# Kernel tuning notes

Hardware: AMD Instinct MI355X
Metric: run time of the kernel (lower is better)

Reference implementation:

```python
import jax, jax.numpy as jnp
import numpy as np

N, E, D, H, Z = 20000, 320000, 512, 512, 128
SCALING_FACTOR = 1.0


def setup_inputs() -> dict:
    key = jax.random.key(0)
    ks = jax.random.split(key, 12)
    def glorot(k, fi, fo):
        lim = float(np.sqrt(6.0 / (fi + fo)))
        return jax.random.uniform(k, (fi, fo), jnp.float32, -lim, lim)
    return {
        "x": jax.random.normal(ks[0], (N, D), jnp.float32),
        "edge_index": jax.random.randint(ks[1], (2, E), 0, N, jnp.int32),
        "eps": jax.random.normal(ks[2], (N, Z), jnp.float32),
        "W1": glorot(ks[3], D, H), "b1": jnp.zeros((H,), jnp.float32),
        "W2": glorot(ks[4], H, H), "b2": jnp.zeros((H,), jnp.float32),
        "Wmu": glorot(ks[5], H, Z), "bmu": jnp.zeros((Z,), jnp.float32),
        "Wlv": glorot(ks[6], H, Z), "blv": jnp.zeros((Z,), jnp.float32),
    }


def reference(x, edge_index, eps, W1, b1, W2, b2, Wmu, bmu, Wlv, blv):
    n = x.shape[0]
    src, dst = edge_index[0], edge_index[1]
    # GCN symmetric normalization with added self-loops (PyG GCNConv default)
    deg = jax.ops.segment_sum(jnp.ones(src.shape[0], x.dtype), dst, num_segments=n) + 1.0
    dinv = jax.lax.rsqrt(deg)                      # deg^{-1/2}, deg >= 1
    edge_coef = dinv[src] * dinv[dst]              # [E]
    self_coef = dinv * dinv                        # [N] self-loop weight

    def gcn(h, W, b):
        h = h @ W                                  # linear first, then propagate
        agg = jax.ops.segment_sum(h[src] * edge_coef[:, None], dst, num_segments=n)
        return agg + self_coef[:, None] * h + b

    # hidden layer 0: relu -> dropout(eval=identity) -> L2 normalize * scaling
    h = jax.nn.relu(gcn(x, W1, b1))
    h = h / jnp.maximum(jnp.linalg.norm(h, axis=1, keepdims=True), 1e-12) * SCALING_FACTOR
    # hidden layer 1 (last): relu only
    h = jax.nn.relu(gcn(h, W2, b2))
    # GaussianSample: GCN heads for mu / log_var, reparameterized sample
    mu = gcn(h, Wmu, bmu)
    log_var = gcn(h, Wlv, blv)
    z = mu + eps * jnp.exp(0.5 * log_var)
    return z, mu, log_var
```

## Files before the change

### kernel.cpp

```cpp
#include <hip/hip_runtime.h>

typedef __bf16 bf16x8 __attribute__((ext_vector_type(8)));
typedef __bf16 bf16x4 __attribute__((ext_vector_type(4)));
typedef float  f32x4  __attribute__((ext_vector_type(4)));
typedef float  f32x2  __attribute__((ext_vector_type(2)));

#define GLDS16(g, l) __builtin_amdgcn_global_load_lds( \
    (const __attribute__((address_space(1))) void*)(g), \
    (__attribute__((address_space(3))) void*)(l), 16, 0, 0)

#define FP8_SCALE 64.0f
#define FP8_INV   (1.0f / 64.0f)

__device__ __forceinline__ unsigned char fp8_of_f32(float v) {
  return (unsigned char)(__builtin_amdgcn_cvt_pk_fp8_f32(v, v, 0, false) & 0xff);
}
__device__ __forceinline__ void dec4(unsigned int u, float* o) {
  f32x2 lo = __builtin_amdgcn_cvt_pk_f32_fp8(u, false);
  f32x2 hi = __builtin_amdgcn_cvt_pk_f32_fp8(u, true);
  o[0] = lo[0]; o[1] = lo[1]; o[2] = hi[0]; o[3] = hi[1];
}


#define CNT_BLKS 640
#define WT_BLKS  640

__global__ __launch_bounds__(256) void prep_kernel(
    const int* __restrict__ dstv, int* __restrict__ cnt, int E,
    const float* __restrict__ x, __bf16* __restrict__ xb,
    const float* __restrict__ W1, const float* __restrict__ W2,
    const float* __restrict__ Wmu, const float* __restrict__ Wlv,
    __bf16* __restrict__ w1t, __bf16* __restrict__ w2t, __bf16* __restrict__ wct) {
  const int b = blockIdx.x;
  if (b < CNT_BLKS) {
    int idx = b * 256 + threadIdx.x;
    for (int e = idx; e < E; e += CNT_BLKS * 256) atomicAdd(&cnt[dstv[e]], 1);
  } else if (b < CNT_BLKS + WT_BLKS) {
    __shared__ float tile[32][33];
    int t = b - CNT_BLKS;
    const float* S; __bf16* D; int kt, ntl, drow, snw;
    if (t < 256)      { S = W1;  D = w1t; kt = t & 15;        ntl = t >> 4;        drow = ntl * 32;       snw = 512; }
    else if (t < 512) { int u = t - 256; S = W2;  D = w2t; kt = u & 15; ntl = u >> 4; drow = ntl * 32;       snw = 512; }
    else if (t < 576) { int u = t - 512; S = Wmu; D = wct; kt = u & 15; ntl = u >> 4; drow = ntl * 32;       snw = 128; }
    else              { int u = t - 576; S = Wlv; D = wct; kt = u & 15; ntl = u >> 4; drow = 128 + ntl * 32; snw = 128; }
    const int k0 = kt * 32, n0 = ntl * 32;
    const int r = threadIdx.x >> 5, c = threadIdx.x & 31;
    #pragma unroll
    for (int p = 0; p < 4; p++)
      tile[r + p * 8][c] = S[(k0 + r + p * 8) * snw + n0 + c];
    __syncthreads();
    #pragma unroll
    for (int p = 0; p < 4; p++)
      D[(drow + r + p * 8) * 512 + k0 + c] = (__bf16)tile[c][r + p * 8];
  } else {
    int id = (b - CNT_BLKS - WT_BLKS) * 256 + threadIdx.x;
    if (id < 2560000) {
      float4 v = ((const float4*)x)[id];
      bf16x4 o; o[0] = (__bf16)v.x; o[1] = (__bf16)v.y; o[2] = (__bf16)v.z; o[3] = (__bf16)v.w;
      ((bf16x4*)xb)[id] = o;
    }
  }
}


__global__ __launch_bounds__(1024) void scan1_kernel(const int* __restrict__ cnt,
                                                     int* __restrict__ rowptr,
                                                     float* __restrict__ dinv,
                                                     int* __restrict__ bsum, int n) {
  __shared__ int wsum[16];
  const int t = threadIdx.x, b = blockIdx.x;
  const int gid = b * 1024 + t;
  const int lane = t & 63, w = t >> 6;
  int val = (gid < n) ? cnt[gid] : 0;
  if (gid < n) dinv[gid] = rsqrtf((float)val + 1.0f);
  int incl = val;
  #pragma unroll
  for (int off = 1; off < 64; off <<= 1) {
    int u = __shfl_up(incl, off);
    if (lane >= off) incl += u;
  }
  if (lane == 63) wsum[w] = incl;
  __syncthreads();
  if (w == 0) {
    int v = (lane < 16) ? wsum[lane] : 0;
    int iv = v;
    #pragma unroll
    for (int off = 1; off < 16; off <<= 1) {
      int u = __shfl_up(iv, off);
      if (lane >= off) iv += u;
    }
    if (lane < 16) wsum[lane] = iv - v;
    if (lane == 15) bsum[b] = iv;
  }
  __syncthreads();
  if (gid < n) rowptr[gid] = wsum[w] + incl - val;
}

__global__ __launch_bounds__(1024) void scan23_kernel(int* __restrict__ rowptr,
                                                      const int* __restrict__ bsum,
                                                      int n, int nb) {
  __shared__ int off_s;
  const int b = blockIdx.x;
  if (threadIdx.x == 0) {
    int run = 0;
    for (int i = 0; i < b; i++) run += bsum[i];
    off_s = run;
    if (b == nb - 1) rowptr[n] = run + bsum[b];
  }
  __syncthreads();
  int gid = b * 1024 + threadIdx.x;
  if (gid < n) rowptr[gid] += off_s;
}


__device__ __forceinline__ void gemm_tile(int orig, int nb,
                                          const __bf16* __restrict__ A,
                                          const __bf16* __restrict__ Bt,
                                          unsigned char* __restrict__ C,
                                          int M, int N, int K, int ntiles_n) {
  __shared__ __align__(16) __bf16 sA[2][128 * 32];
  __shared__ __align__(16) __bf16 sB[2][128 * 32];
  const int q = nb >> 3, r = nb & 7;
  const int xcd = orig & 7, sub = orig >> 3;
  const int pos = (xcd < r) ? (xcd * (q + 1) + sub) : (r * (q + 1) + (xcd - r) * q + sub);
  const int m0 = (pos / ntiles_n) * 128, n0 = (pos % ntiles_n) * 128;

  const int tid = threadIdx.x;
  const int wave = tid >> 6, lane = tid & 63;
  const int wr = wave >> 1, wc = wave & 1;
  f32x4 acc[4][4] = {};
  const int srow = lane >> 2;
  const int sg   = (lane & 3) ^ ((srow >> 1) & 3);
  const int nt = K >> 5;

  auto STAGE = [&](int bb, int k0) {
    #pragma unroll
    for (int c = 0; c < 2; ++c) {
      int chunk = wave * 2 + c;
      int row = chunk * 16 + srow;
      int ga = m0 + row; if (ga >= M) ga = M - 1;
      GLDS16(A  + (long)ga * K         + k0 + sg * 8, sA[bb] + chunk * 512);
      GLDS16(Bt + (long)(n0 + row) * K + k0 + sg * 8, sB[bb] + chunk * 512);
    }
  };

  STAGE(0, 0);
  for (int t = 0; t < nt; ++t) {
    const int cur = t & 1;
    if (t + 1 < nt) {
      STAGE(cur ^ 1, (t + 1) << 5);
      asm volatile("s_waitcnt vmcnt(4)" ::: "memory");
    } else {
      asm volatile("s_waitcnt vmcnt(0)" ::: "memory");
    }
    __builtin_amdgcn_s_barrier();
    __builtin_amdgcn_sched_barrier(0);

    const int fr = lane & 15, gbase = lane >> 4;
    const int gs = gbase ^ ((fr >> 1) & 3);
    bf16x8 af[4], bfr[4];
    #pragma unroll
    for (int mi = 0; mi < 4; mi++)
      af[mi] = *(const bf16x8*)(sA[cur] + (wr * 64 + mi * 16 + fr) * 32 + gs * 8);
    #pragma unroll
    for (int ni = 0; ni < 4; ni++)
      bfr[ni] = *(const bf16x8*)(sB[cur] + (wc * 64 + ni * 16 + fr) * 32 + gs * 8);
    #pragma unroll
    for (int mi = 0; mi < 4; mi++)
      #pragma unroll
      for (int ni = 0; ni < 4; ni++)
        acc[mi][ni] = __builtin_amdgcn_mfma_f32_16x16x32_bf16(af[mi], bfr[ni], acc[mi][ni], 0, 0, 0);
    asm volatile("s_waitcnt lgkmcnt(0)" ::: "memory");
    __builtin_amdgcn_sched_barrier(0);
    __builtin_amdgcn_s_barrier();
  }

  const int crow0 = (lane >> 4) * 4, ccol = lane & 15;
  #pragma unroll
  for (int mi = 0; mi < 4; mi++)
    #pragma unroll
    for (int ni = 0; ni < 4; ni++)
      #pragma unroll
      for (int r2 = 0; r2 < 4; r2++) {
        int row = m0 + wr * 64 + mi * 16 + crow0 + r2;
        if (row < M)
          C[(long)row * N + n0 + wc * 64 + ni * 16 + ccol] =
              fp8_of_f32(acc[mi][ni][r2] * FP8_SCALE);
      }
}

__global__ __launch_bounds__(256, 4) void gemm_bt(const __bf16* __restrict__ A,
                                                  const __bf16* __restrict__ Bt,
                                                  unsigned char* __restrict__ C,
                                                  int M, int N, int K, int ntiles_n, int ngb) {
  gemm_tile(blockIdx.x, ngb, A, Bt, C, M, N, K, ntiles_n);
}

__global__ __launch_bounds__(256, 4) void gemm1_fill_kernel(
    const __bf16* __restrict__ A, const __bf16* __restrict__ Bt,
    unsigned char* __restrict__ C, int M, int N, int K, int ntiles_n, int ngb,
    const int* __restrict__ src, const int* __restrict__ dstv,
    const int* __restrict__ rowptr, int* __restrict__ cur,
    const float* __restrict__ dinv, int2* __restrict__ csr_pack, int E) {
  if (blockIdx.x < (unsigned)ngb) {
    gemm_tile(blockIdx.x, ngb, A, Bt, C, M, N, K, ntiles_n);
  } else {
    int idx = (blockIdx.x - ngb) * 256 + threadIdx.x;
    int stride = (gridDim.x - ngb) * 256;
    for (int e = idx; e < E; e += stride) {
      int s = src[e], d = dstv[e];
      int slot = rowptr[d] + atomicAdd(&cur[d], 1);
      int2 p; p.x = s; p.y = __float_as_int(dinv[s] * dinv[d] * FP8_INV);
      csr_pack[slot] = p;
    }
  }
}


template<int EPL> struct LSel;
template<> struct LSel<8> { typedef uint2 T; };
template<> struct LSel<4> { typedef unsigned int T; };

template<int EPL, int MODE>
__global__ __launch_bounds__(512) void prop_kernel(
    const unsigned char* __restrict__ Cin, const int* __restrict__ rowptr,
    const int2* __restrict__ csr_pack,
    const float* __restrict__ dinv, const float* __restrict__ bias,
    const float* __restrict__ bmu, const float* __restrict__ blv,
    const float* __restrict__ eps,
    __bf16* __restrict__ hout, float* __restrict__ zout, int n) {
  constexpr int F = EPL * 64;
  typedef typename LSel<EPL>::T VecT;
  const int lane = threadIdx.x & 63;
  const int i = blockIdx.x * (blockDim.x >> 6) + (threadIdx.x >> 6);
  if (i >= n) return;
  const unsigned char* __restrict__ Clane = Cin + lane * EPL;

  auto decAll = [&](VecT v, float* o) {
    if constexpr (EPL == 8) { dec4(v.x, o); dec4(v.y, o + 4); }
    else                    { dec4(v, o); }
  };

  float acc[EPL];
  {
    const float di = dinv[i];
    const float sc = di * di * FP8_INV;
    VecT v = *(const VecT*)(Clane + (size_t)i * F);
    float dv[EPL];
    decAll(v, dv);
    #pragma unroll
    for (int j = 0; j < EPL; j++) acc[j] = sc * dv[j];
  }
  int e = rowptr[i];
  const int e1 = rowptr[i + 1];
  for (; e + 8 <= e1; e += 8) {
    int2 p[8];
    #pragma unroll
    for (int q = 0; q < 8; q++) p[q] = csr_pack[e + q];
    VecT v[8];
    #pragma unroll
    for (int q = 0; q < 8; q++) v[q] = *(const VecT*)(Clane + (size_t)p[q].x * F);
    #pragma unroll
    for (int q = 0; q < 8; q++) {
      float c = __int_as_float(p[q].y);
      float dv[EPL];
      decAll(v[q], dv);
      #pragma unroll
      for (int j = 0; j < EPL; j++) acc[j] += c * dv[j];
    }
  }
  for (; e + 4 <= e1; e += 4) {
    int2 p[4];
    #pragma unroll
    for (int q = 0; q < 4; q++) p[q] = csr_pack[e + q];
    VecT v[4];
    #pragma unroll
    for (int q = 0; q < 4; q++) v[q] = *(const VecT*)(Clane + (size_t)p[q].x * F);
    #pragma unroll
    for (int q = 0; q < 4; q++) {
      float c = __int_as_float(p[q].y);
      float dv[EPL];
      decAll(v[q], dv);
      #pragma unroll
      for (int j = 0; j < EPL; j++) acc[j] += c * dv[j];
    }
  }
  for (; e < e1; ++e) {
    int2 p = csr_pack[e];
    float c = __int_as_float(p.y);
    VecT v = *(const VecT*)(Clane + (size_t)p.x * F);
    float dv[EPL];
    decAll(v, dv);
    #pragma unroll
    for (int j = 0; j < EPL; j++) acc[j] += c * dv[j];
  }

  if constexpr (MODE == 0 || MODE == 1) {
    float ss = 0.f;
    #pragma unroll
    for (int j = 0; j < EPL; j++) {
      acc[j] += bias[lane * EPL + j];
      acc[j] = fmaxf(acc[j], 0.f);
      ss += acc[j] * acc[j];
    }
    float scale = 1.f;
    if constexpr (MODE == 0) {
      #pragma unroll
      for (int off = 32; off > 0; off >>= 1) ss += __shfl_xor(ss, off);
      scale = 1.f / fmaxf(sqrtf(ss), 1e-12f);
    }
    bf16x8 o;
    #pragma unroll
    for (int j = 0; j < EPL; j++) o[j] = (__bf16)(acc[j] * scale);
    *(bf16x8*)(hout + (size_t)i * 512 + lane * EPL) = o;
  } else {
    const bool ismu = lane < 32;
    const int cb4 = (ismu ? lane : lane - 32) * 4;
    float v[4];
    #pragma unroll
    for (int j = 0; j < 4; j++) v[j] = acc[j] + (ismu ? bmu[cb4 + j] : blv[cb4 + j]);
    const size_t NZ = (size_t)n * 128;
    float* dstp = ismu ? (zout + NZ + (size_t)i * 128 + cb4)
                       : (zout + 2 * NZ + (size_t)i * 128 + cb4);
    float4 st; st.x = v[0]; st.y = v[1]; st.z = v[2]; st.w = v[3];
    *(float4*)dstp = st;
    float ov[4];
    #pragma unroll
    for (int j = 0; j < 4; j++) ov[j] = __shfl_xor(v[j], 32);
    if (ismu) {
      float4 ev = *(const float4*)(eps + (size_t)i * 128 + cb4);
      float4 zs;
      zs.x = v[0] + ev.x * expf(0.5f * ov[0]);
      zs.y = v[1] + ev.y * expf(0.5f * ov[1]);
      zs.z = v[2] + ev.z * expf(0.5f * ov[2]);
      zs.w = v[3] + ev.w * expf(0.5f * ov[3]);
      *(float4*)(zout + (size_t)i * 128 + cb4) = zs;
    }
  }
}


extern "C" void kernel_launch(void* const* d_in, const int* in_sizes, int n_in,
                              void* d_out, int out_size, void* d_ws, size_t ws_size,
                              hipStream_t stream) {
  const float* x   = (const float*)d_in[0];
  const int*   ei  = (const int*)d_in[1];
  const float* eps = (const float*)d_in[2];
  const float* W1  = (const float*)d_in[3];
  const float* b1  = (const float*)d_in[4];
  const float* W2  = (const float*)d_in[5];
  const float* b2  = (const float*)d_in[6];
  const float* Wmu = (const float*)d_in[7];
  const float* bmu = (const float*)d_in[8];
  const float* Wlv = (const float*)d_in[9];
  const float* blv = (const float*)d_in[10];
  float* out = (float*)d_out;

  const int N = 20000, E = 320000, D = 512, H = 512, Z = 128;
  const int* src = ei;
  const int* dst = ei + E;
  const int NB = (N + 1023) / 1024;

  char* p = (char*)d_ws;
  auto alloc = [&](size_t bytes) { char* r = p; p += (bytes + 255) & ~(size_t)255; return r; };
  int*    cnt      = (int*)alloc((size_t)N * 4);
  int*    cur      = (int*)alloc((size_t)N * 4);
  int*    rowptr   = (int*)alloc((size_t)(N + 1) * 4);
  float*  dinv     = (float*)alloc((size_t)N * 4);
  int*    bsum     = (int*)alloc((size_t)NB * 4);
  int2*   csr_pack = (int2*)alloc((size_t)E * 8);
  __bf16* xb  = (__bf16*)alloc((size_t)N * D * 2);
  __bf16* hb  = (__bf16*)alloc((size_t)N * H * 2);
  unsigned char* cb = (unsigned char*)alloc((size_t)N * H);
  __bf16* w1t = (__bf16*)alloc((size_t)D * H * 2);
  __bf16* w2t = (__bf16*)alloc((size_t)H * H * 2);
  __bf16* wct = (__bf16*)alloc((size_t)2 * Z * H * 2);

  hipMemsetAsync(cnt, 0, ((size_t)N * 4 + 255 & ~(size_t)255) + (size_t)N * 4, stream);

  prep_kernel<<<CNT_BLKS + WT_BLKS + 10000, 256, 0, stream>>>(
      dst, cnt, E, x, xb, W1, W2, Wmu, Wlv, w1t, w2t, wct);
  scan1_kernel<<<NB, 1024, 0, stream>>>(cnt, rowptr, dinv, bsum, N);
  scan23_kernel<<<NB, 1024, 0, stream>>>(rowptr, bsum, N, NB);

  const int NGB1 = ((N + 127) / 128) * (H / 128);
  gemm1_fill_kernel<<<NGB1 + 1250, 256, 0, stream>>>(
      xb, w1t, cb, N, H, D, H / 128, NGB1,
      src, dst, rowptr, cur, dinv, csr_pack, E);
  prop_kernel<8, 0><<<2500, 512, 0, stream>>>(cb, rowptr, csr_pack, dinv,
                                              b1, nullptr, nullptr, nullptr, hb, nullptr, N);
  gemm_bt<<<NGB1, 256, 0, stream>>>(hb, w2t, cb, N, H, H, H / 128, NGB1);
  prop_kernel<8, 1><<<2500, 512, 0, stream>>>(cb, rowptr, csr_pack, dinv,
                                              b2, nullptr, nullptr, nullptr, xb, nullptr, N);
  const int NGB3 = ((N + 127) / 128) * ((2 * Z) / 128);
  gemm_bt<<<NGB3, 256, 0, stream>>>(xb, wct, cb, N, 2 * Z, H, (2 * Z) / 128, NGB3);
  prop_kernel<4, 2><<<2500, 512, 0, stream>>>(cb, rowptr, csr_pack, dinv,
                                              nullptr, bmu, blv, eps, nullptr, out, N);
}
```

Before: 182.2 us.

## Fuse all stages into one cooperative persistent kernel with grid syncs

Replaces the sequence of separate launches (prep, count, scans, gemms, propagations) with one cooperative mega-kernel that loops persistently over work and separates phases with grid.sync, keeping a multi-kernel fallback. The memset is folded into the prep phase. The intent is to remove per-launch overhead and inter-kernel gaps. In exchange, occupancy is capped at the cooperative grid size (at most 1024 blocks), the GEMM runs as grid-strided tiles, grid-wide barriers add their own cost, and the edge fill may no longer overlap with the GEMM if the grid is too small.

```diff
diff --git a/kernel.cpp b/kernel.cpp
--- a/kernel.cpp
+++ b/kernel.cpp
@@ -1,4 +1,7 @@
 #include <hip/hip_runtime.h>
+#include <hip/hip_cooperative_groups.h>
+
+namespace cg = cooperative_groups;
 
 typedef __bf16 bf16x8 __attribute__((ext_vector_type(8)));
 typedef __bf16 bf16x4 __attribute__((ext_vector_type(4)));
@@ -12,6 +15,13 @@
 #define FP8_SCALE 64.0f
 #define FP8_INV   (1.0f / 64.0f)
 
+#define MN    20000
+#define ME    320000
+#define NGB1  628
+#define NGB3  314
+#define SCB   80
+#define SMEM_B (32768 + 32)
+
 __device__ __forceinline__ unsigned char fp8_of_f32(float v) {
   return (unsigned char)(__builtin_amdgcn_cvt_pk_fp8_f32(v, v, 0, false) & 0xff);
 }
@@ -21,105 +31,27 @@
   o[0] = lo[0]; o[1] = lo[1]; o[2] = hi[0]; o[3] = hi[1];
 }
 
-
-#define CNT_BLKS 640
-#define WT_BLKS  640
-
-__global__ __launch_bounds__(256) void prep_kernel(
-    const int* __restrict__ dstv, int* __restrict__ cnt, int E,
-    const float* __restrict__ x, __bf16* __restrict__ xb,
-    const float* __restrict__ W1, const float* __restrict__ W2,
-    const float* __restrict__ Wmu, const float* __restrict__ Wlv,
-    __bf16* __restrict__ w1t, __bf16* __restrict__ w2t, __bf16* __restrict__ wct) {
-  const int b = blockIdx.x;
-  if (b < CNT_BLKS) {
-    int idx = b * 256 + threadIdx.x;
-    for (int e = idx; e < E; e += CNT_BLKS * 256) atomicAdd(&cnt[dstv[e]], 1);
-  } else if (b < CNT_BLKS + WT_BLKS) {
-    __shared__ float tile[32][33];
-    int t = b - CNT_BLKS;
-    const float* S; __bf16* D; int kt, ntl, drow, snw;
-    if (t < 256)      { S = W1;  D = w1t; kt = t & 15;        ntl = t >> 4;        drow = ntl * 32;       snw = 512; }
-    else if (t < 512) { int u = t - 256; S = W2;  D = w2t; kt = u & 15; ntl = u >> 4; drow = ntl * 32;       snw = 512; }
-    else if (t < 576) { int u = t - 512; S = Wmu; D = wct; kt = u & 15; ntl = u >> 4; drow = ntl * 32;       snw = 128; }
-    else              { int u = t - 576; S = Wlv; D = wct; kt = u & 15; ntl = u >> 4; drow = 128 + ntl * 32; snw = 128; }
-    const int k0 = kt * 32, n0 = ntl * 32;
-    const int r = threadIdx.x >> 5, c = threadIdx.x & 31;
-    #pragma unroll
-    for (int p = 0; p < 4; p++)
-      tile[r + p * 8][c] = S[(k0 + r + p * 8) * snw + n0 + c];
-    __syncthreads();
-    #pragma unroll
-    for (int p = 0; p < 4; p++)
-      D[(drow + r + p * 8) * 512 + k0 + c] = (__bf16)tile[c][r + p * 8];
-  } else {
-    int id = (b - CNT_BLKS - WT_BLKS) * 256 + threadIdx.x;
-    if (id < 2560000) {
-      float4 v = ((const float4*)x)[id];
-      bf16x4 o; o[0] = (__bf16)v.x; o[1] = (__bf16)v.y; o[2] = (__bf16)v.z; o[3] = (__bf16)v.w;
-      ((bf16x4*)xb)[id] = o;
-    }
-  }
-}
-
-
-__global__ __launch_bounds__(1024) void scan1_kernel(const int* __restrict__ cnt,
-                                                     int* __restrict__ rowptr,
-                                                     float* __restrict__ dinv,
-                                                     int* __restrict__ bsum, int n) {
-  __shared__ int wsum[16];
-  const int t = threadIdx.x, b = blockIdx.x;
-  const int gid = b * 1024 + t;
-  const int lane = t & 63, w = t >> 6;
-  int val = (gid < n) ? cnt[gid] : 0;
-  if (gid < n) dinv[gid] = rsqrtf((float)val + 1.0f);
-  int incl = val;
-  #pragma unroll
-  for (int off = 1; off < 64; off <<= 1) {
-    int u = __shfl_up(incl, off);
-    if (lane >= off) incl += u;
-  }
-  if (lane == 63) wsum[w] = incl;
-  __syncthreads();
-  if (w == 0) {
-    int v = (lane < 16) ? wsum[lane] : 0;
-    int iv = v;
-    #pragma unroll
-    for (int off = 1; off < 16; off <<= 1) {
-      int u = __shfl_up(iv, off);
-      if (lane >= off) iv += u;
-    }
-    if (lane < 16) wsum[lane] = iv - v;
-    if (lane == 15) bsum[b] = iv;
-  }
-  __syncthreads();
-  if (gid < n) rowptr[gid] = wsum[w] + incl - val;
-}
-
-__global__ __launch_bounds__(1024) void scan23_kernel(int* __restrict__ rowptr,
-                                                      const int* __restrict__ bsum,
-                                                      int n, int nb) {
-  __shared__ int off_s;
-  const int b = blockIdx.x;
-  if (threadIdx.x == 0) {
-    int run = 0;
-    for (int i = 0; i < b; i++) run += bsum[i];
-    off_s = run;
-    if (b == nb - 1) rowptr[n] = run + bsum[b];
-  }
-  __syncthreads();
-  int gid = b * 1024 + threadIdx.x;
-  if (gid < n) rowptr[gid] += off_s;
-}
+struct MegaArgs {
+  const int* src; const int* dstv;
+  int* cnt; int* cur; int* rowptr; float* dinv; int* bsum;
+  int2* csr_pack;
+  const float* x; __bf16* xb;
+  const float* W1; const float* W2; const float* Wmu; const float* Wlv;
+  __bf16* w1t; __bf16* w2t; __bf16* wct;
+  unsigned char* cb; __bf16* hb;
+  const float* b1; const float* b2; const float* bmu; const float* blv;
+  const float* eps; float* zout;
+};
 
 
 __device__ __forceinline__ void gemm_tile(int orig, int nb,
                                           const __bf16* __restrict__ A,
                                           const __bf16* __restrict__ Bt,
                                           unsigned char* __restrict__ C,
-                                          int M, int N, int K, int ntiles_n) {
-  __shared__ __align__(16) __bf16 sA[2][128 * 32];
-  __shared__ __align__(16) __bf16 sB[2][128 * 32];
+                                          int M, int N, int K, int ntiles_n,
+                                          char* smem) {
+  __bf16* sA[2] = { (__bf16*)smem, (__bf16*)smem + 128 * 32 };
+  __bf16* sB[2] = { (__bf16*)smem + 2 * 128 * 32, (__bf16*)smem + 3 * 128 * 32 };
   const int q = nb >> 3, r = nb & 7;
   const int xcd = orig & 7, sub = orig >> 3;
   const int pos = (xcd < r) ? (xcd * (q + 1) + sub) : (r * (q + 1) + (xcd - r) * q + sub);
@@ -189,31 +121,118 @@
       }
 }
 
-__global__ __launch_bounds__(256, 4) void gemm_bt(const __bf16* __restrict__ A,
-                                                  const __bf16* __restrict__ Bt,
-                                                  unsigned char* __restrict__ C,
-                                                  int M, int N, int K, int ntiles_n, int ngb) {
-  gemm_tile(blockIdx.x, ngb, A, Bt, C, M, N, K, ntiles_n);
-}
-
-__global__ __launch_bounds__(256, 4) void gemm1_fill_kernel(
-    const __bf16* __restrict__ A, const __bf16* __restrict__ Bt,
-    unsigned char* __restrict__ C, int M, int N, int K, int ntiles_n, int ngb,
-    const int* __restrict__ src, const int* __restrict__ dstv,
-    const int* __restrict__ rowptr, int* __restrict__ cur,
-    const float* __restrict__ dinv, int2* __restrict__ csr_pack, int E) {
-  if (blockIdx.x < (unsigned)ngb) {
-    gemm_tile(blockIdx.x, ngb, A, Bt, C, M, N, K, ntiles_n);
+
+__device__ void ph_prep(const MegaArgs& a, char* smem) {
+  float (*tile)[33] = (float(*)[33])smem;
+  const int b = blockIdx.x, t = threadIdx.x;
+  const int G = gridDim.x;
+  const int gtid = b * 256 + t, gsz = G * 256;
+  for (int i = gtid; i < MN; i += gsz) { a.cnt[i] = 0; a.cur[i] = 0; }
+  for (int tt = b; tt < 640; tt += G) {
+    const float* S; __bf16* D; int kt, ntl, drow, snw;
+    if (tt < 256)      { S = a.W1;  D = a.w1t; kt = tt & 15;  ntl = tt >> 4; drow = ntl * 32;       snw = 512; }
+    else if (tt < 512) { int u = tt - 256; S = a.W2;  D = a.w2t; kt = u & 15; ntl = u >> 4; drow = ntl * 32;       snw = 512; }
+    else if (tt < 576) { int u = tt - 512; S = a.Wmu; D = a.wct; kt = u & 15; ntl = u >> 4; drow = ntl * 32;       snw = 128; }
+    else               { int u = tt - 576; S = a.Wlv; D = a.wct; kt = u & 15; ntl = u >> 4; drow = 128 + ntl * 32; snw = 128; }
+    const int k0 = kt * 32, n0 = ntl * 32;
+    const int r = t >> 5, c = t & 31;
+    #pragma unroll
+    for (int p = 0; p < 4; p++)
+      tile[r + p * 8][c] = S[(k0 + r + p * 8) * snw + n0 + c];
+    __syncthreads();
+    #pragma unroll
+    for (int p = 0; p < 4; p++)
+      D[(drow + r + p * 8) * 512 + k0 + c] = (__bf16)tile[c][r + p * 8];
+    __syncthreads();
+  }
+  for (int id = gtid; id < 2560000; id += gsz) {
+    float4 v = ((const float4*)a.x)[id];
+    bf16x4 o; o[0] = (__bf16)v.x; o[1] = (__bf16)v.y; o[2] = (__bf16)v.z; o[3] = (__bf16)v.w;
+    ((bf16x4*)a.xb)[id] = o;
+  }
+}
+
+__device__ void ph_count(const MegaArgs& a) {
+  const int gtid = blockIdx.x * 256 + threadIdx.x, gsz = gridDim.x * 256;
+  for (int e = gtid; e < ME; e += gsz) atomicAdd(&a.cnt[a.dstv[e]], 1);
+}
+
+__device__ void ph_scan1(const MegaArgs& a, char* smem) {
+  int* ssc = (int*)(smem + 32768);
+  const int t = threadIdx.x;
+  const int lane = t & 63, w = t >> 6;
+  for (int sb = blockIdx.x; sb < SCB; sb += gridDim.x) {
+    const int gid = sb * 256 + t;
+    int val = (gid < MN) ? a.cnt[gid] : 0;
+    if (gid < MN) a.dinv[gid] = rsqrtf((float)val + 1.0f);
+    int incl = val;
+    #pragma unroll
+    for (int off = 1; off < 64; off <<= 1) {
+      int u = __shfl_up(incl, off);
+      if (lane >= off) incl += u;
+    }
+    if (lane == 63) ssc[w] = incl;
+    __syncthreads();
+    if (t == 0) {
+      int s = 0;
+      #pragma unroll
+      for (int j = 0; j < 4; j++) { int tmp = ssc[j]; ssc[j] = s; s += tmp; }
+      a.bsum[sb] = s;
+    }
+    __syncthreads();
+    if (gid < MN) a.rowptr[gid] = ssc[w] + incl - val;
+    __syncthreads();
+  }
+}
+
+__device__ void ph_scan23(const MegaArgs& a, char* smem) {
+  int* ssc = (int*)(smem + 32768);
+  const int t = threadIdx.x;
+  for (int sb = blockIdx.x; sb < SCB; sb += gridDim.x) {
+    if (t == 0) {
+      int run = 0;
+      for (int i = 0; i < sb; i++) run += a.bsum[i];
+      ssc[4] = run;
+      if (sb == SCB - 1) a.rowptr[MN] = run + a.bsum[sb];
+    }
+    __syncthreads();
+    const int gid = sb * 256 + t;
+    if (gid < MN) a.rowptr[gid] += ssc[4];
+    __syncthreads();
+  }
+}
+
+__device__ __forceinline__ void fill_edges(const MegaArgs& a, int idx, int stride) {
+  for (int e = idx; e < ME; e += stride) {
+    int s = a.src[e], d = a.dstv[e];
+    int slot = a.rowptr[d] + atomicAdd(&a.cur[d], 1);
+    int2 pp; pp.x = s; pp.y = __float_as_int(a.dinv[s] * a.dinv[d] * FP8_INV);
+    a.csr_pack[slot] = pp;
+  }
+}
+
+__device__ void ph_gemm1_fill(const MegaArgs& a, char* smem) {
+  const int G = gridDim.x, b = blockIdx.x;
+  if (G >= NGB1 + 64) {
+    if (b < NGB1)
+      gemm_tile(b, NGB1, a.xb, a.w1t, a.cb, MN, 512, 512, 4, smem);
+    else
+      fill_edges(a, (b - NGB1) * 256 + threadIdx.x, (G - NGB1) * 256);
   } else {
-    int idx = (blockIdx.x - ngb) * 256 + threadIdx.x;
-    int stride = (gridDim.x - ngb) * 256;
-    for (int e = idx; e < E; e += stride) {
-      int s = src[e], d = dstv[e];
-      int slot = rowptr[d] + atomicAdd(&cur[d], 1);
-      int2 p; p.x = s; p.y = __float_as_int(dinv[s] * dinv[d] * FP8_INV);
-      csr_pack[slot] = p;
-    }
-  }
+    for (int tl = b; tl < NGB1; tl += G)
+      gemm_tile(tl, NGB1, a.xb, a.w1t, a.cb, MN, 512, 512, 4, smem);
+    fill_edges(a, b * 256 + threadIdx.x, G * 256);
+  }
+}
+
+__device__ void ph_gemm2(const MegaArgs& a, char* smem) {
+  for (int tl = blockIdx.x; tl < NGB1; tl += gridDim.x)
+    gemm_tile(tl, NGB1, a.hb, a.w2t, a.cb, MN, 512, 512, 4, smem);
+}
+
+__device__ void ph_gemm3(const MegaArgs& a, char* smem) {
+  for (int tl = blockIdx.x; tl < NGB3; tl += gridDim.x)
+    gemm_tile(tl, NGB3, a.xb, a.wct, a.cb, MN, 256, 512, 2, smem);
 }
 
 
@@ -222,18 +241,13 @@
 template<> struct LSel<4> { typedef unsigned int T; };
 
 template<int EPL, int MODE>
-__global__ __launch_bounds__(512) void prop_kernel(
-    const unsigned char* __restrict__ Cin, const int* __restrict__ rowptr,
-    const int2* __restrict__ csr_pack,
-    const float* __restrict__ dinv, const float* __restrict__ bias,
-    const float* __restrict__ bmu, const float* __restrict__ blv,
-    const float* __restrict__ eps,
-    __bf16* __restrict__ hout, float* __restrict__ zout, int n) {
+__device__ void prop_phase(const MegaArgs& a, const unsigned char* __restrict__ Cin,
+                           const float* __restrict__ bias, __bf16* __restrict__ hout) {
   constexpr int F = EPL * 64;
   typedef typename LSel<EPL>::T VecT;
   const int lane = threadIdx.x & 63;
-  const int i = blockIdx.x * (blockDim.x >> 6) + (threadIdx.x >> 6);
-  if (i >= n) return;
+  const int w = threadIdx.x >> 6;
+  const int nw = gridDim.x * 4;
   const unsigned char* __restrict__ Clane = Cin + lane * EPL;
 
   auto decAll = [&](VecT v, float* o) {
@@ -241,125 +255,140 @@
     else                    { dec4(v, o); }
   };
 
-  float acc[EPL];
-  {
-    const float di = dinv[i];
-    const float sc = di * di * FP8_INV;
-    VecT v = *(const VecT*)(Clane + (size_t)i * F);
-    float dv[EPL];
-    decAll(v, dv);
-    #pragma unroll
-    for (int j = 0; j < EPL; j++) acc[j] = sc * dv[j];
-  }
-  int e = rowptr[i];
-  const int e1 = rowptr[i + 1];
-  for (; e + 8 <= e1; e += 8) {
-    int2 p[8];
-    #pragma unroll
-    for (int q = 0; q < 8; q++) p[q] = csr_pack[e + q];
-    VecT v[8];
-    #pragma unroll
-    for (int q = 0; q < 8; q++) v[q] = *(const VecT*)(Clane + (size_t)p[q].x * F);
-    #pragma unroll
-    for (int q = 0; q < 8; q++) {
-      float c = __int_as_float(p[q].y);
+  for (int i = blockIdx.x * 4 + w; i < MN; i += nw) {
+    float acc[EPL];
+    {
+      const float di = a.dinv[i];
+      const float sc = di * di * FP8_INV;
+      VecT v = *(const VecT*)(Clane + (size_t)i * F);
       float dv[EPL];
-      decAll(v[q], dv);
+      decAll(v, dv);
+      #pragma unroll
+      for (int j = 0; j < EPL; j++) acc[j] = sc * dv[j];
+    }
+    int e = a.rowptr[i];
+    const int e1 = a.rowptr[i + 1];
+    for (; e + 8 <= e1; e += 8) {
+      int2 p[8];
+      #pragma unroll
+      for (int qq = 0; qq < 8; qq++) p[qq] = a.csr_pack[e + qq];
+      VecT v[8];
+      #pragma unroll
+      for (int qq = 0; qq < 8; qq++) v[qq] = *(const VecT*)(Clane + (size_t)p[qq].x * F);
+      #pragma unroll
+      for (int qq = 0; qq < 8; qq++) {
+        float c = __int_as_float(p[qq].y);
+        float dv[EPL];
+        decAll(v[qq], dv);
+        #pragma unroll
+        for (int j = 0; j < EPL; j++) acc[j] += c * dv[j];
+      }
+    }
+    for (; e + 4 <= e1; e += 4) {
+      int2 p[4];
+      #pragma unroll
+      for (int qq = 0; qq < 4; qq++) p[qq] = a.csr_pack[e + qq];
+      VecT v[4];
+      #pragma unroll
+      for (int qq = 0; qq < 4; qq++) v[qq] = *(const VecT*)(Clane + (size_t)p[qq].x * F);
+      #pragma unroll
+      for (int qq = 0; qq < 4; qq++) {
+        float c = __int_as_float(p[qq].y);
+        float dv[EPL];
+        decAll(v[qq], dv);
+        #pragma unroll
+        for (int j = 0; j < EPL; j++) acc[j] += c * dv[j];
+      }
+    }
+    for (; e < e1; ++e) {
+      int2 p = a.csr_pack[e];
+      float c = __int_as_float(p.y);
+      VecT v = *(const VecT*)(Clane + (size_t)p.x * F);
+      float dv[EPL];
+      decAll(v, dv);
       #pragma unroll
       for (int j = 0; j < EPL; j++) acc[j] += c * dv[j];
     }
-  }
-  for (; e + 4 <= e1; e += 4) {
-    int2 p[4];
-    #pragma unroll
-    for (int q = 0; q < 4; q++) p[q] = csr_pack[e + q];
-    VecT v[4];
-    #pragma unroll
-    for (int q = 0; q < 4; q++) v[q] = *(const VecT*)(Clane + (size_t)p[q].x * F);
-    #pragma unroll
-    for (int q = 0; q < 4; q++) {
-      float c = __int_as_float(p[q].y);
-      float dv[EPL];
-      decAll(v[q], dv);
-      #pragma unroll
-      for (int j = 0; j < EPL; j++) acc[j] += c * dv[j];
-    }
-  }
-  for (; e < e1; ++e) {
-    int2 p = csr_pack[e];
-    float c = __int_as_float(p.y);
-    VecT v = *(const VecT*)(Clane + (size_t)p.x * F);
-    float dv[EPL];
-    decAll(v, dv);
-    #pragma unroll
-    for (int j = 0; j < EPL; j++) acc[j] += c * dv[j];
-  }
-
-  if constexpr (MODE == 0 || MODE == 1) {
-    float ss = 0.f;
-    #pragma unroll
-    for (int j = 0; j < EPL; j++) {
-      acc[j] += bias[lane * EPL + j];
-      acc[j] = fmaxf(acc[j], 0.f);
-      ss += acc[j] * acc[j];
-    }
-    float scale = 1.f;
-    if constexpr (MODE == 0) {
-      #pragma unroll
-      for (int off = 32; off > 0; off >>= 1) ss += __shfl_xor(ss, off);
-      scale = 1.f / fmaxf(sqrtf(ss), 1e-12f);
-    }
-    bf16x8 o;
-    #pragma unroll
-    for (int j = 0; j < EPL; j++) o[j] = (__bf16)(acc[j] * scale);
-    *(bf16x8*)(hout + (size_t)i * 512 + lane * EPL) = o;
-  } else {
-    const bool ismu = lane < 32;
-    const int cb4 = (ismu ? lane : lane - 32) * 4;
-    float v[4];
-    #pragma unroll
-    for (int j = 0; j < 4; j++) v[j] = acc[j] + (ismu ? bmu[cb4 + j] : blv[cb4 + j]);
-    const size_t NZ = (size_t)n * 128;
-    float* dstp = ismu ? (zout + NZ + (size_t)i * 128 + cb4)
-                       : (zout + 2 * NZ + (size_t)i * 128 + cb4);
-    float4 st; st.x = v[0]; st.y = v[1]; st.z = v[2]; st.w = v[3];
-    *(float4*)dstp = st;
-    float ov[4];
-    #pragma unroll
-    for (int j = 0; j < 4; j++) ov[j] = __shfl_xor(v[j], 32);
-    if (ismu) {
-      float4 ev = *(const float4*)(eps + (size_t)i * 128 + cb4);
-      float4 zs;
-      zs.x = v[0] + ev.x * expf(0.5f * ov[0]);
-      zs.y = v[1] + ev.y * expf(0.5f * ov[1]);
-      zs.z = v[2] + ev.z * expf(0.5f * ov[2]);
-      zs.w = v[3] + ev.w * expf(0.5f * ov[3]);
-      *(float4*)(zout + (size_t)i * 128 + cb4) = zs;
-    }
-  }
-}
+
+    if constexpr (MODE == 0 || MODE == 1) {
+      float ss = 0.f;
+      #pragma unroll
+      for (int j = 0; j < EPL; j++) {
+        acc[j] += bias[lane * EPL + j];
+        acc[j] = fmaxf(acc[j], 0.f);
+        ss += acc[j] * acc[j];
+      }
+      float scale = 1.f;
+      if constexpr (MODE == 0) {
+        #pragma unroll
+        for (int off = 32; off > 0; off >>= 1) ss += __shfl_xor(ss, off);
+        scale = 1.f / fmaxf(sqrtf(ss), 1e-12f);
+      }
+      bf16x8 o;
+      #pragma unroll
+      for (int j = 0; j < EPL; j++) o[j] = (__bf16)(acc[j] * scale);
+      *(bf16x8*)(hout + (size_t)i * 512 + lane * EPL) = o;
+    } else {
+      const bool ismu = lane < 32;
+      const int cb4 = (ismu ? lane : lane - 32) * 4;
+      float v[4];
+      #pragma unroll
+      for (int j = 0; j < 4; j++) v[j] = acc[j] + (ismu ? a.bmu[cb4 + j] : a.blv[cb4 + j]);
+      const size_t NZ = (size_t)MN * 128;
+      float* dstp = ismu ? (a.zout + NZ + (size_t)i * 128 + cb4)
+                         : (a.zout + 2 * NZ + (size_t)i * 128 + cb4);
+      float4 st; st.x = v[0]; st.y = v[1]; st.z = v[2]; st.w = v[3];
+      *(float4*)dstp = st;
+      float ov[4];
+      #pragma unroll
+      for (int j = 0; j < 4; j++) ov[j] = __shfl_xor(v[j], 32);
+      if (ismu) {
+        float4 ev = *(const float4*)(a.eps + (size_t)i * 128 + cb4);
+        float4 zs;
+        zs.x = v[0] + ev.x * expf(0.5f * ov[0]);
+        zs.y = v[1] + ev.y * expf(0.5f * ov[1]);
+        zs.z = v[2] + ev.z * expf(0.5f * ov[2]);
+        zs.w = v[3] + ev.w * expf(0.5f * ov[3]);
+        *(float4*)(a.zout + (size_t)i * 128 + cb4) = zs;
+      }
+    }
+  }
+}
+
+
+__global__ void __launch_bounds__(256) mega_kernel(MegaArgs a) {
+  cg::grid_group grid = cg::this_grid();
+  __shared__ __align__(16) char smem[SMEM_B];
+
+  ph_prep(a, smem);                                   grid.sync();
+  ph_count(a);                                        grid.sync();
+  ph_scan1(a, smem);                                  grid.sync();
+  ph_scan23(a, smem);                                 grid.sync();
+  ph_gemm1_fill(a, smem);                             grid.sync();
+  prop_phase<8, 0>(a, a.cb, a.b1, a.hb);              grid.sync();
+  ph_gemm2(a, smem);                                  grid.sync();
+  prop_phase<8, 1>(a, a.cb, a.b2, a.xb);              grid.sync();
+  ph_gemm3(a, smem);                                  grid.sync();
+  prop_phase<4, 2>(a, a.cb, nullptr, nullptr);
+}
+
+
+__global__ void __launch_bounds__(256) k_prep(MegaArgs a)   { __shared__ __align__(16) char s[SMEM_B]; ph_prep(a, s); }
+__global__ void __launch_bounds__(256) k_count(MegaArgs a)  { ph_count(a); }
+__global__ void __launch_bounds__(256) k_scan1(MegaArgs a)  { __shared__ __align__(16) char s[SMEM_B]; ph_scan1(a, s); }
+__global__ void __launch_bounds__(256) k_scan23(MegaArgs a) { __shared__ __align__(16) char s[SMEM_B]; ph_scan23(a, s); }
+__global__ void __launch_bounds__(256) k_g1fill(MegaArgs a) { __shared__ __align__(16) char s[SMEM_B]; ph_gemm1_fill(a, s); }
+__global__ void __launch_bounds__(256) k_gemm2(MegaArgs a)  { __shared__ __align__(16) char s[SMEM_B]; ph_gemm2(a, s); }
+__global__ void __launch_bounds__(256) k_gemm3(MegaArgs a)  { __shared__ __align__(16) char s[SMEM_B]; ph_gemm3(a, s); }
+__global__ void __launch_bounds__(256) k_prop0(MegaArgs a)  { prop_phase<8, 0>(a, a.cb, a.b1, a.hb); }
+__global__ void __launch_bounds__(256) k_prop1(MegaArgs a)  { prop_phase<8, 1>(a, a.cb, a.b2, a.xb); }
+__global__ void __launch_bounds__(256) k_prop2(MegaArgs a)  { prop_phase<4, 2>(a, a.cb, nullptr, nullptr); }
 
 
 extern "C" void kernel_launch(void* const* d_in, const int* in_sizes, int n_in,
                               void* d_out, int out_size, void* d_ws, size_t ws_size,
                               hipStream_t stream) {
-  const float* x   = (const float*)d_in[0];
-  const int*   ei  = (const int*)d_in[1];
-  const float* eps = (const float*)d_in[2];
-  const float* W1  = (const float*)d_in[3];
-  const float* b1  = (const float*)d_in[4];
-  const float* W2  = (const float*)d_in[5];
-  const float* b2  = (const float*)d_in[6];
-  const float* Wmu = (const float*)d_in[7];
-  const float* bmu = (const float*)d_in[8];
-  const float* Wlv = (const float*)d_in[9];
-  const float* blv = (const float*)d_in[10];
-  float* out = (float*)d_out;
-
   const int N = 20000, E = 320000, D = 512, H = 512, Z = 128;
-  const int* src = ei;
-  const int* dst = ei + E;
-  const int NB = (N + 1023) / 1024;
 
   char* p = (char*)d_ws;
   auto alloc = [&](size_t bytes) { char* r = p; p += (bytes + 255) & ~(size_t)255; return r; };
@@ -367,7 +396,7 @@
   int*    cur      = (int*)alloc((size_t)N * 4);
   int*    rowptr   = (int*)alloc((size_t)(N + 1) * 4);
   float*  dinv     = (float*)alloc((size_t)N * 4);
-  int*    bsum     = (int*)alloc((size_t)NB * 4);
+  int*    bsum     = (int*)alloc((size_t)SCB * 4);
   int2*   csr_pack = (int2*)alloc((size_t)E * 8);
   __bf16* xb  = (__bf16*)alloc((size_t)N * D * 2);
   __bf16* hb  = (__bf16*)alloc((size_t)N * H * 2);
@@ -376,24 +405,41 @@
   __bf16* w2t = (__bf16*)alloc((size_t)H * H * 2);
   __bf16* wct = (__bf16*)alloc((size_t)2 * Z * H * 2);
 
-  hipMemsetAsync(cnt, 0, ((size_t)N * 4 + 255 & ~(size_t)255) + (size_t)N * 4, stream);
-
-  prep_kernel<<<CNT_BLKS + WT_BLKS + 10000, 256, 0, stream>>>(
-      dst, cnt, E, x, xb, W1, W2, Wmu, Wlv, w1t, w2t, wct);
-  scan1_kernel<<<NB, 1024, 0, stream>>>(cnt, rowptr, dinv, bsum, N);
-  scan23_kernel<<<NB, 1024, 0, stream>>>(rowptr, bsum, N, NB);
-
-  const int NGB1 = ((N + 127) / 128) * (H / 128);
-  gemm1_fill_kernel<<<NGB1 + 1250, 256, 0, stream>>>(
-      xb, w1t, cb, N, H, D, H / 128, NGB1,
-      src, dst, rowptr, cur, dinv, csr_pack, E);
-  prop_kernel<8, 0><<<2500, 512, 0, stream>>>(cb, rowptr, csr_pack, dinv,
-                                              b1, nullptr, nullptr, nullptr, hb, nullptr, N);
-  gemm_bt<<<NGB1, 256, 0, stream>>>(hb, w2t, cb, N, H, H, H / 128, NGB1);
-  prop_kernel<8, 1><<<2500, 512, 0, stream>>>(cb, rowptr, csr_pack, dinv,
-                                              b2, nullptr, nullptr, nullptr, xb, nullptr, N);
-  const int NGB3 = ((N + 127) / 128) * ((2 * Z) / 128);
-  gemm_bt<<<NGB3, 256, 0, stream>>>(xb, wct, cb, N, 2 * Z, H, (2 * Z) / 128, NGB3);
-  prop_kernel<4, 2><<<2500, 512, 0, stream>>>(cb, rowptr, csr_pack, dinv,
-                                              nullptr, bmu, blv, eps, nullptr, out, N);
-}
+  MegaArgs a;
+  a.src = (const int*)d_in[1];
+  a.dstv = (const int*)d_in[1] + E;
+  a.cnt = cnt; a.cur = cur; a.rowptr = rowptr; a.dinv = dinv; a.bsum = bsum;
+  a.csr_pack = csr_pack;
+  a.x = (const float*)d_in[0]; a.xb = xb;
+  a.W1 = (const float*)d_in[3]; a.W2 = (const float*)d_in[5];
+  a.Wmu = (const float*)d_in[7]; a.Wlv = (const float*)d_in[9];
+  a.w1t = w1t; a.w2t = w2t; a.wct = wct;
+  a.cb = cb; a.hb = hb;
+  a.b1 = (const float*)d_in[4]; a.b2 = (const float*)d_in[6];
+  a.bmu = (const float*)d_in[8]; a.blv = (const float*)d_in[10];
+  a.eps = (const float*)d_in[2]; a.zout = (float*)d_out;
+
+  int maxAct = 0;
+  hipError_t qerr = hipOccupancyMaxActiveBlocksPerMultiprocessor(
+      &maxAct, (const void*)mega_kernel, 256, 0);
+  long coopGrid = (qerr == hipSuccess) ? (long)maxAct * 256 : 0;
+  hipError_t lerr = hipErrorUnknown;
+  if (coopGrid >= 512) {
+    if (coopGrid > 1024) coopGrid = 1024;
+    void* kargs[] = { (void*)&a };
+    lerr = hipLaunchCooperativeKernel((const void*)mega_kernel,
+                                      dim3((unsigned)coopGrid), dim3(256), kargs, 0, stream);
+  }
+  if (lerr != hipSuccess) {
+    k_prep  <<<4096, 256, 0, stream>>>(a);
+    k_count <<<1250, 256, 0, stream>>>(a);
+    k_scan1 <<<SCB,  256, 0, stream>>>(a);
+    k_scan23<<<SCB,  256, 0, stream>>>(a);
+    k_g1fill<<<NGB1 + 256, 256, 0, stream>>>(a);
+    k_prop0 <<<2500, 256, 0, stream>>>(a);
+    k_gemm2 <<<NGB1, 256, 0, stream>>>(a);
+    k_prop1 <<<2500, 256, 0, stream>>>(a);
+    k_gemm3 <<<NGB3, 256, 0, stream>>>(a);
+    k_prop2 <<<2500, 256, 0, stream>>>(a);
+  }
+}
```

New measurement: 192.7 us. 1.06x slower.
